# Kernel tuning notes

Hardware: AMD Instinct MI355X
Metric: run time of the kernel (lower is better)

## Reference

```python
import jax, jax.numpy as jnp
import numpy as np

BETA = 8.0  # inverse temperature from __init__


def setup_inputs() -> dict:
    key = jax.random.key(0)
    k1, k2 = jax.random.split(key)
    B, N, D = 2048, 100000, 512
    query = jax.random.normal(k1, (B, D), dtype=jnp.float32)
    memory = jax.random.normal(k2, (N, D), dtype=jnp.float32)
    return {"query": query, "memory": memory, "steps": 2}


def reference(query, memory, steps):
    # Iterative modern-Hopfield retrieval (normalize=False path):
    # x <- sigmoid(softmax(beta * x @ M^T) @ M), repeated `steps` times.
    x = query.astype(jnp.float32)
    for _ in range(int(steps)):
        logits = BETA * jnp.einsum('bd,nd->bn', x, memory)   # [B, N]
        attn = jax.nn.softmax(logits, axis=-1)               # [B, N]
        x = jax.nn.sigmoid(jnp.einsum('bn,nd->bd', attn, memory))  # [B, D]
    return x
```

## Files before the change

### kernel.cpp

```cpp
#include <hip/hip_runtime.h>
#include <hip/hip_bf16.h>


#define B_ROWS 2048
#define DDIM   512
#define NTOT   100000
#define NPAD   100096
#define QBLKS  16
#define NTILES 782
#define PTILES 32
#define CAP    2048
#define SCAP   512
#define MARGIN 35.0f
#define WCUT   15.0f

typedef int   i32x4 __attribute__((ext_vector_type(4)));
typedef float f32x4 __attribute__((ext_vector_type(4)));

__device__ inline unsigned encf(float f){
  unsigned u = __float_as_uint(f);
  return (u & 0x80000000u) ? ~u : (u | 0x80000000u);
}
__device__ inline float decf(unsigned u){
  unsigned v = (u & 0x80000000u) ? (u ^ 0x80000000u) : ~u;
  return __uint_as_float(v);
}
__device__ inline void llds16(const void* g, void* l){
  __builtin_amdgcn_global_load_lds(
      (const __attribute__((address_space(1))) unsigned int*)(unsigned long long)g,
      (__attribute__((address_space(3))) unsigned int*)(unsigned long long)l,
      16, 0, 0);
}
__device__ inline unsigned q4(float a, float b, float c, float d, float mult){
  int qa = (int)fmaxf(-127.f, fminf(127.f, rintf(a*mult)));
  int qb = (int)fmaxf(-127.f, fminf(127.f, rintf(b*mult)));
  int qc = (int)fmaxf(-127.f, fminf(127.f, rintf(c*mult)));
  int qd = (int)fmaxf(-127.f, fminf(127.f, rintf(d*mult)));
  return (qa & 0xff) | ((qb & 0xff) << 8) | ((qc & 0xff) << 16) | ((qd & 0xff) << 24);
}

__global__ void cvt_i8(const float* __restrict__ src, signed char* __restrict__ dst,
                       long nsrc, long ndst, float mult){
  long i = ((long)blockIdx.x * blockDim.x + threadIdx.x) * 16;
  if (i >= ndst) return;
  uint4 o;
  if (i < nsrc){
    const float4* p = (const float4*)(src + i);
    float4 a = p[0], b = p[1], c = p[2], d = p[3];
    o.x = q4(a.x, a.y, a.z, a.w, mult);
    o.y = q4(b.x, b.y, b.z, b.w, mult);
    o.z = q4(c.x, c.y, c.z, c.w, mult);
    o.w = q4(d.x, d.y, d.z, d.w, mult);
  } else { o.x = o.y = o.z = o.w = 0u; }
  *(uint4*)(dst + i) = o;
}

__global__ void init_stats(unsigned* __restrict__ m0u, unsigned* __restrict__ cnt){
  int i = blockIdx.x * blockDim.x + threadIdx.x;
  if (i < B_ROWS){ m0u[i] = 0u; cnt[i] = 0u; }
}

template<int MODE>
__launch_bounds__(256, 2)
__global__ void gemm_tile(const signed char* __restrict__ A,
                          const signed char* __restrict__ Bm,
                          unsigned* __restrict__ m0u,
                          unsigned* __restrict__ cnt,
                          int* __restrict__ cand,
                          float dq){
  __shared__ signed char Alds[128*64];
  __shared__ signed char Blds[128*64];
  __shared__ float tt[128];

  const int qblk = blockIdx.x, nblk = blockIdx.y;
  const int tid  = threadIdx.x;
  const int lane = tid & 63, wave = tid >> 6;
  const int wr = wave >> 1, wc = wave & 1;
  const int quad = lane >> 4, l15 = lane & 15;

  if (MODE == 1 && tid < 128) tt[tid] = decf(m0u[qblk*128 + tid]) - MARGIN;

  const signed char* gA = A  + (size_t)(qblk*128 + wave*16 + (lane>>2))*DDIM + (lane&3)*16;
  const signed char* gB = Bm + (size_t)(nblk*128 + wave*16 + (lane>>2))*DDIM + (lane&3)*16;
  signed char* lA0 = Alds + wave*1024;
  signed char* lA1 = Alds + 4096 + wave*1024;
  signed char* lB0 = Blds + wave*1024;
  signed char* lB1 = Blds + 4096 + wave*1024;

  const int aoff = (wr*64 + l15)*64 + quad*16;
  const int boff = (wc*64 + l15)*64 + quad*16;

  i32x4 acc[4][4] = {};

  for (int kb = 0; kb < DDIM/64; ++kb){
    __syncthreads();
    llds16(gA,           lA0);
    llds16(gA + 64*DDIM, lA1);
    llds16(gB,           lB0);
    llds16(gB + 64*DDIM, lB1);
    gA += 64; gB += 64;
    __syncthreads();
    i32x4 af[4], bfr[4];
    #pragma unroll
    for (int i = 0; i < 4; i++) af[i]  = *(const i32x4*)(Alds + aoff + i*1024);
    #pragma unroll
    for (int j = 0; j < 4; j++) bfr[j] = *(const i32x4*)(Blds + boff + j*1024);
    #pragma unroll
    for (int i = 0; i < 4; i++)
      #pragma unroll
      for (int j = 0; j < 4; j++)
        acc[i][j] = __builtin_amdgcn_mfma_i32_16x16x64_i8(af[i], bfr[j], acc[i][j], 0, 0, 0);
  }

  if (MODE == 0){
    #pragma unroll
    for (int i = 0; i < 4; i++){
      #pragma unroll
      for (int r = 0; r < 4; r++){
        float v = fmaxf(fmaxf((float)acc[i][0][r], (float)acc[i][1][r]),
                        fmaxf((float)acc[i][2][r], (float)acc[i][3][r])) * dq;
        #pragma unroll
        for (int m = 1; m < 16; m <<= 1) v = fmaxf(v, __shfl_xor(v, m));
        if (l15 == 0){
          int row = qblk*128 + wr*64 + i*16 + quad*4 + r;
          atomicMax(&m0u[row], encf(v));
        }
      }
    }
  } else {
    const int nbase = nblk*128 + wc*64 + l15;
    #pragma unroll
    for (int i = 0; i < 4; i++){
      #pragma unroll
      for (int r = 0; r < 4; r++){
        const int lrow = wr*64 + i*16 + quad*4 + r;
        const float t = tt[lrow];
        #pragma unroll
        for (int j = 0; j < 4; j++){
          float v = (float)acc[i][j][r] * dq;
          int n = nbase + j*16;
          if (v > t && n < NTOT){
            int q = qblk*128 + lrow;
            unsigned pos = atomicAdd(&cnt[q], 1u);
            if (pos < CAP) cand[(size_t)q*CAP + pos] = n;
          }
        }
      }
    }
  }
}

__global__ void finalize_row(const float* __restrict__ xin, const float* __restrict__ M,
                             const int* __restrict__ cand, const unsigned* __restrict__ cnt,
                             float* __restrict__ xout){
  __shared__ float xs[DDIM];
  __shared__ float lc[CAP];
  __shared__ int   sv[SCAP];
  __shared__ float mred[4];
  __shared__ int   ns;
  const int q = blockIdx.x, tid = threadIdx.x;
  const int wave = tid >> 6, lane = tid & 63;
  xs[tid]       = xin[(size_t)q*DDIM + tid];
  xs[tid + 256] = xin[(size_t)q*DDIM + 256 + tid];
  if (tid == 0) ns = 0;
  const unsigned cq = cnt[q];
  const int c0 = (int)(cq < (unsigned)CAP ? cq : (unsigned)CAP);
  __syncthreads();

  for (int c = wave; c < c0; c += 4){
    const float* Mr = M + (size_t)cand[(size_t)q*CAP + c]*DDIM;
    float s = 0.f;
    #pragma unroll
    for (int k = 0; k < 8; k++) s += xs[lane + 64*k] * Mr[lane + 64*k];
    #pragma unroll
    for (int o = 32; o; o >>= 1) s += __shfl_xor(s, o);
    if (lane == 0) lc[c] = 8.0f * s;
  }
  __syncthreads();

  float m = -3.0e38f;
  for (int c = tid; c < c0; c += 256) m = fmaxf(m, lc[c]);
  #pragma unroll
  for (int o = 32; o; o >>= 1) m = fmaxf(m, __shfl_xor(m, o));
  if (lane == 0) mred[wave] = m;
  __syncthreads();
  m = fmaxf(fmaxf(mred[0], mred[1]), fmaxf(mred[2], mred[3]));

  for (int c = tid; c < c0; c += 256){
    if (lc[c] > m - WCUT){
      int p = atomicAdd(&ns, 1);
      if (p < SCAP) sv[p] = c;
    }
  }
  __syncthreads();
  const int nsv = ns < SCAP ? ns : SCAP;

  float Z = 0.f, a0 = 0.f, a1 = 0.f;
  for (int i = 0; i < nsv; i++){
    const int c = sv[i];
    const float w = expf(lc[c] - m);
    const float* Mr = M + (size_t)cand[(size_t)q*CAP + c]*DDIM;
    Z  += w;
    a0 += w * Mr[tid];
    a1 += w * Mr[tid + 256];
  }
  xout[(size_t)q*DDIM + tid]       = 1.f/(1.f + expf(-a0/Z));
  xout[(size_t)q*DDIM + tid + 256] = 1.f/(1.f + expf(-a1/Z));
}

extern "C" void kernel_launch(void* const* d_in, const int* in_sizes, int n_in,
                              void* d_out, int out_size, void* d_ws, size_t ws_size,
                              hipStream_t stream){
  const float* query = (const float*)d_in[0];
  const float* M     = (const float*)d_in[1];
  float* out = (float*)d_out;

  char* w = (char*)d_ws;
  size_t off = 0;
  signed char* Bq   = (signed char*)(w + off); off += (size_t)NPAD*DDIM;
  signed char* Aq   = (signed char*)(w + off); off += (size_t)B_ROWS*DDIM;
  float*       xbuf = (float*)(w + off);       off += (size_t)B_ROWS*DDIM*4;
  unsigned*    m0u  = (unsigned*)(w + off);    off += (size_t)B_ROWS*4;
  unsigned*    cnt  = (unsigned*)(w + off);    off += (size_t)B_ROWS*4;
  int*         cand = (int*)(w + off);         off += (size_t)B_ROWS*CAP*4;
  if (ws_size < off) return;

  const float MCLIP = 4.0f;
  cvt_i8<<<(long)NPAD*DDIM/16/256, 256, 0, stream>>>(M, Bq, (long)NTOT*DDIM, (long)NPAD*DDIM,
                                                     127.0f/MCLIP);

  for (int step = 0; step < 2; ++step){
    const float* x = step ? (const float*)xbuf : query;
    float*       y = step ? out : xbuf;
    const float ACLIP = step ? 8.0f : 40.0f;
    const float multA = 8.0f * 127.0f / ACLIP;
    const float dq    = (ACLIP/127.0f) * (MCLIP/127.0f);
    init_stats<<<8, 256, 0, stream>>>(m0u, cnt);
    cvt_i8<<<(long)B_ROWS*DDIM/16/256, 256, 0, stream>>>(x, Aq, (long)B_ROWS*DDIM,
                                                         (long)B_ROWS*DDIM, multA);
    gemm_tile<0><<<dim3(QBLKS, PTILES), 256, 0, stream>>>(Aq, Bq, m0u, cnt, cand, dq);
    gemm_tile<1><<<dim3(QBLKS, NTILES), 256, 0, stream>>>(Aq, Bq, m0u, cnt, cand, dq);
    finalize_row<<<B_ROWS, 256, 0, stream>>>(x, M, cand, cnt, y);
  }
}
```

Baseline: 693.1 us.

## Fuse max prepass into filter GEMM with running threshold and register-resident A

Removes the separate 32-tile max-estimation GEMM launch. The filter kernel now computes each row's tile max, applies atomicMax, and derives its candidate threshold from the returned running max combined with the local max. The A operand is preloaded into registers for all K, and B is double-buffered in LDS so each K step needs one barrier instead of two. Early tiles see a looser threshold, which may push more candidates through, risks hitting CAP, and adds atomic traffic. Holding A in registers also raises VGPR pressure.

```diff
diff --git a/kernel.cpp b/kernel.cpp
--- a/kernel.cpp
+++ b/kernel.cpp
@@ -8,14 +8,12 @@
 #define NPAD   100096
 #define QBLKS  16
 #define NTILES 782
-#define PTILES 32
 #define CAP    2048
 #define SCAP   512
 #define MARGIN 35.0f
 #define WCUT   15.0f
 
 typedef int   i32x4 __attribute__((ext_vector_type(4)));
-typedef float f32x4 __attribute__((ext_vector_type(4)));
 
 __device__ inline unsigned encf(float f){
   unsigned u = __float_as_uint(f);
@@ -60,17 +58,14 @@
   if (i < B_ROWS){ m0u[i] = 0u; cnt[i] = 0u; }
 }
 
-template<int MODE>
 __launch_bounds__(256, 2)
-__global__ void gemm_tile(const signed char* __restrict__ A,
-                          const signed char* __restrict__ Bm,
-                          unsigned* __restrict__ m0u,
-                          unsigned* __restrict__ cnt,
-                          int* __restrict__ cand,
-                          float dq){
-  __shared__ signed char Alds[128*64];
-  __shared__ signed char Blds[128*64];
-  __shared__ float tt[128];
+__global__ void gemm_filter(const signed char* __restrict__ A,
+                            const signed char* __restrict__ Bm,
+                            unsigned* __restrict__ m0u,
+                            unsigned* __restrict__ cnt,
+                            int* __restrict__ cand,
+                            float dq){
+  __shared__ signed char Blds[2*128*64];
 
   const int qblk = blockIdx.x, nblk = blockIdx.y;
   const int tid  = threadIdx.x;
@@ -78,72 +73,66 @@
   const int wr = wave >> 1, wc = wave & 1;
   const int quad = lane >> 4, l15 = lane & 15;
 
-  if (MODE == 1 && tid < 128) tt[tid] = decf(m0u[qblk*128 + tid]) - MARGIN;
-
-  const signed char* gA = A  + (size_t)(qblk*128 + wave*16 + (lane>>2))*DDIM + (lane&3)*16;
+  i32x4 ap[32];
+  {
+    const signed char* pa = A + (size_t)(qblk*128 + wr*64 + l15)*DDIM + quad*16;
+    #pragma unroll
+    for (int kb = 0; kb < 8; kb++)
+      #pragma unroll
+      for (int i = 0; i < 4; i++)
+        ap[kb*4+i] = *(const i32x4*)(pa + (size_t)i*16*DDIM + kb*64);
+  }
+
   const signed char* gB = Bm + (size_t)(nblk*128 + wave*16 + (lane>>2))*DDIM + (lane&3)*16;
-  signed char* lA0 = Alds + wave*1024;
-  signed char* lA1 = Alds + 4096 + wave*1024;
-  signed char* lB0 = Blds + wave*1024;
-  signed char* lB1 = Blds + 4096 + wave*1024;
-
-  const int aoff = (wr*64 + l15)*64 + quad*16;
   const int boff = (wc*64 + l15)*64 + quad*16;
 
   i32x4 acc[4][4] = {};
 
-  for (int kb = 0; kb < DDIM/64; ++kb){
+  llds16(gB,           Blds + wave*1024);
+  llds16(gB + 64*DDIM, Blds + 4096 + wave*1024);
+  gB += 64;
+
+  #pragma unroll
+  for (int kb = 0; kb < 8; kb++){
     __syncthreads();
-    llds16(gA,           lA0);
-    llds16(gA + 64*DDIM, lA1);
-    llds16(gB,           lB0);
-    llds16(gB + 64*DDIM, lB1);
-    gA += 64; gB += 64;
-    __syncthreads();
-    i32x4 af[4], bfr[4];
-    #pragma unroll
-    for (int i = 0; i < 4; i++) af[i]  = *(const i32x4*)(Alds + aoff + i*1024);
-    #pragma unroll
-    for (int j = 0; j < 4; j++) bfr[j] = *(const i32x4*)(Blds + boff + j*1024);
+    const int cur = (kb & 1) * 8192;
+    if (kb < 7){
+      const int nxt = 8192 - cur;
+      llds16(gB,           Blds + nxt + wave*1024);
+      llds16(gB + 64*DDIM, Blds + nxt + 4096 + wave*1024);
+      gB += 64;
+    }
+    i32x4 bfr[4];
+    #pragma unroll
+    for (int j = 0; j < 4; j++) bfr[j] = *(const i32x4*)(Blds + cur + boff + j*1024);
     #pragma unroll
     for (int i = 0; i < 4; i++)
       #pragma unroll
       for (int j = 0; j < 4; j++)
-        acc[i][j] = __builtin_amdgcn_mfma_i32_16x16x64_i8(af[i], bfr[j], acc[i][j], 0, 0, 0);
-  }
-
-  if (MODE == 0){
-    #pragma unroll
-    for (int i = 0; i < 4; i++){
-      #pragma unroll
-      for (int r = 0; r < 4; r++){
-        float v = fmaxf(fmaxf((float)acc[i][0][r], (float)acc[i][1][r]),
-                        fmaxf((float)acc[i][2][r], (float)acc[i][3][r])) * dq;
-        #pragma unroll
-        for (int m = 1; m < 16; m <<= 1) v = fmaxf(v, __shfl_xor(v, m));
-        if (l15 == 0){
-          int row = qblk*128 + wr*64 + i*16 + quad*4 + r;
-          atomicMax(&m0u[row], encf(v));
-        }
-      }
-    }
-  } else {
-    const int nbase = nblk*128 + wc*64 + l15;
-    #pragma unroll
-    for (int i = 0; i < 4; i++){
-      #pragma unroll
-      for (int r = 0; r < 4; r++){
-        const int lrow = wr*64 + i*16 + quad*4 + r;
-        const float t = tt[lrow];
-        #pragma unroll
-        for (int j = 0; j < 4; j++){
-          float v = (float)acc[i][j][r] * dq;
-          int n = nbase + j*16;
-          if (v > t && n < NTOT){
-            int q = qblk*128 + lrow;
-            unsigned pos = atomicAdd(&cnt[q], 1u);
-            if (pos < CAP) cand[(size_t)q*CAP + pos] = n;
-          }
+        acc[i][j] = __builtin_amdgcn_mfma_i32_16x16x64_i8(ap[kb*4+i], bfr[j], acc[i][j], 0, 0, 0);
+  }
+
+  const int nbase = nblk*128 + wc*64 + l15;
+  #pragma unroll
+  for (int i = 0; i < 4; i++){
+    #pragma unroll
+    for (int r = 0; r < 4; r++){
+      float hm = fmaxf(fmaxf((float)acc[i][0][r], (float)acc[i][1][r]),
+                       fmaxf((float)acc[i][2][r], (float)acc[i][3][r])) * dq;
+      #pragma unroll
+      for (int m = 1; m < 16; m <<= 1) hm = fmaxf(hm, __shfl_xor(hm, m));
+      const int row = qblk*128 + wr*64 + i*16 + quad*4 + r;
+      unsigned pre = 0u;
+      if (l15 == 0) pre = atomicMax(&m0u[row], encf(hm));
+      pre = __shfl(pre, quad*16);
+      const float thr = fmaxf(decf(pre), hm) - MARGIN;
+      #pragma unroll
+      for (int j = 0; j < 4; j++){
+        float v = (float)acc[i][j][r] * dq;
+        int n = nbase + j*16;
+        if (v > thr && n < NTOT){
+          unsigned pos = atomicAdd(&cnt[row], 1u);
+          if (pos < CAP) cand[(size_t)row*CAP + pos] = n;
         }
       }
     }
@@ -238,8 +227,7 @@
     init_stats<<<8, 256, 0, stream>>>(m0u, cnt);
     cvt_i8<<<(long)B_ROWS*DDIM/16/256, 256, 0, stream>>>(x, Aq, (long)B_ROWS*DDIM,
                                                          (long)B_ROWS*DDIM, multA);
-    gemm_tile<0><<<dim3(QBLKS, PTILES), 256, 0, stream>>>(Aq, Bq, m0u, cnt, cand, dq);
-    gemm_tile<1><<<dim3(QBLKS, NTILES), 256, 0, stream>>>(Aq, Bq, m0u, cnt, cand, dq);
+    gemm_filter<<<dim3(QBLKS, NTILES), 256, 0, stream>>>(Aq, Bq, m0u, cnt, cand, dq);
     finalize_row<<<B_ROWS, 256, 0, stream>>>(x, M, cand, cnt, y);
   }
 }
```

Result: slower. 1.408 ms (+103.1%).
